# Kernel optimization log

Hardware: AMD Instinct MI355X
Metric: run time of the kernel (lower is better)

## Reference

```python
import jax, jax.numpy as jnp
import numpy as np

N = 8192
IOU_THRESH = 0.5
MAX_PROPOSALS = 1000


def setup_inputs() -> dict:
    key = jax.random.key(0)
    k1, k2, k3, k4 = jax.random.split(key, 4)
    # valid xyxy boxes inside a ~1000x1000 image, widths/heights in [1, 101)
    xy1 = jax.random.uniform(k1, (N, 2), dtype=jnp.float32) * 900.0
    wh = jax.random.uniform(k2, (N, 2), dtype=jnp.float32) * 100.0 + 1.0
    boxes = jnp.concatenate([xy1, xy1 + wh], axis=1)  # [N,4] xyxy
    scores = jax.random.uniform(k3, (N,), dtype=jnp.float32)
    return {"boxes": boxes, "scores": scores}


def _nms_keep(boxes, scores, thresh, max_proposals):
    # boxes: [N,4] xyxy (already sorted by descending score)
    x1, y1, x2, y2 = boxes[:, 0], boxes[:, 1], boxes[:, 2], boxes[:, 3]
    area = (x2 - x1) * (y2 - y1)  # [N]
    # pairwise IoU [N,N] (computed once; suppression loop gathers rows)
    xx1 = jnp.maximum(x1[:, None], x1[None, :])
    yy1 = jnp.maximum(y1[:, None], y1[None, :])
    xx2 = jnp.minimum(x2[:, None], x2[None, :])
    yy2 = jnp.minimum(y2[:, None], y2[None, :])
    inter = jnp.clip(xx2 - xx1, 0.0) * jnp.clip(yy2 - yy1, 0.0)
    iou = inter / (area[:, None] + area[None, :] - inter)
    n = boxes.shape[0]
    idx = jnp.arange(n)

    def body(i, keep):
        # box i (if still kept) suppresses later boxes with IoU > thresh
        suppress = keep[i] & (iou[i] > thresh) & (idx > i)
        return keep & ~suppress

    keep = jax.lax.fori_loop(0, n, body, jnp.ones((n,), dtype=bool))
    # truncate to max_proposals surviving boxes (in score order)
    keep = keep & (jnp.cumsum(keep.astype(jnp.int32)) <= max_proposals)
    return keep


def reference(boxes, scores):
    # sort by descending score (boxlist_nms sorts by score_field)
    order = jnp.argsort(-scores)
    b = boxes[order]          # [N,4]
    s = scores[order]         # [N]
    # keep mask is a discrete decision -> computed on stop_gradient inputs
    keep = _nms_keep(jax.lax.stop_gradient(b), jax.lax.stop_gradient(s),
                     IOU_THRESH, MAX_PROPOSALS)
    # fixed-shape output: [N,5] = (x1,y1,x2,y2,score), zeroed where suppressed
    out = jnp.concatenate([b, s[:, None]], axis=1) * keep[:, None].astype(b.dtype)
    return out
```

## Files before the change

kernel.cpp:

```cpp
#include <hip/hip_runtime.h>
#include <hip/hip_bf16.h>

#define N 8192
#define NW 128
#define GR 64
#define GROUPS 128
#define CGR 48
#define MAXP 1000
#define K_E 16
typedef unsigned long long u64;

__device__ float4 g_sboxes[N];
__device__ float  g_sscores[N];
__device__ u64    g_mask[(size_t)N * NW];
__device__ u64    g_diagT[N];
__device__ __attribute__((aligned(8))) unsigned short g_elist[N][K_E];
__device__ int    g_ecnt[N];
__device__ int    g_need_full;

__global__ __launch_bounds__(256) void k_rank2(const float4* __restrict__ boxes,
                                               const float* __restrict__ scores) {
  __shared__ u64 lk[8][1025];
  const int t = threadIdx.x;
  if (blockIdx.x < 32) g_ecnt[blockIdx.x * 256 + t] = 0;
  if (blockIdx.x == 0 && t == 0) g_need_full = 0;
#pragma unroll
  for (int k = 0; k < 32; ++k) {
    int j = t + 256 * k;
    unsigned sb = __float_as_uint(scores[j]);
    lk[j >> 10][j & 1023] = ((u64)(sb ^ 0xFFFFFFFFu) << 32) | (unsigned)j;
  }
  __syncthreads();
  const int row = blockIdx.x * 32 + (t >> 3);
  const int seg = t & 7;
  unsigned sbr = __float_as_uint(scores[row]);
  const u64 ki = ((u64)(sbr ^ 0xFFFFFFFFu) << 32) | (unsigned)row;
  const u64* s = lk[seg];
  int cnt = 0;
#pragma unroll 8
  for (int j = 0; j < 1024; ++j) cnt += (s[j] < ki) ? 1 : 0;
  cnt += __shfl_xor(cnt, 1);
  cnt += __shfl_xor(cnt, 2);
  cnt += __shfl_xor(cnt, 4);
  if (seg == 0) {
    g_sboxes[cnt] = boxes[row];
    g_sscores[cnt] = scores[row];
  }
}

__device__ __forceinline__ void tile_work(int col, int row, int lane,
                                          const float4* cb, u64* sh) {
#pragma clang fp contract(off)
  const int i = row * 64 + lane;
  const int jbase = col * 64;
  float4 bi = g_sboxes[i];
  u64 ov = 0;
  for (int c = 0; c < 64; ++c) {
    float4 bj = cb[c];
    float xx1 = fmaxf(bi.x, bj.x);
    float yy1 = fmaxf(bi.y, bj.y);
    float xx2 = fminf(bi.z, bj.z);
    float yy2 = fminf(bi.w, bj.w);
    bool cand = (xx2 > xx1) && (yy2 > yy1);
    if (cand) ov |= (1ull << c);
  }
  if (col == row) ov &= (lane < 63) ? (~0ull << (lane + 1)) : 0ull;
  float areai = (bi.z - bi.x) * (bi.w - bi.y);
  u64 bits = 0;
  while (ov) {
    int c = __ffsll((long long)ov) - 1;
    ov &= ov - 1;
    float4 bj = cb[c];
    float xx1 = fmaxf(bi.x, bj.x);
    float yy1 = fmaxf(bi.y, bj.y);
    float xx2 = fminf(bi.z, bj.z);
    float yy2 = fminf(bi.w, bj.w);
    float ww = fmaxf(xx2 - xx1, 0.0f);
    float hh = fmaxf(yy2 - yy1, 0.0f);
    float inter = ww * hh;
    float areaj = (bj.z - bj.x) * (bj.w - bj.y);
    float uni = (areai + areaj) - inter;
    float iou = inter / uni;
    if (iou > 0.5f) bits |= (1ull << c);
  }
  if (bits) g_mask[(size_t)i * NW + col] = bits;
  u64 eb = bits;
  while (eb) {
    int c = __ffsll((long long)eb) - 1;
    eb &= eb - 1;
    int slot = atomicAdd(&g_ecnt[i], 1);
    if (slot < K_E) g_elist[i][slot] = (unsigned short)(jbase + c);
  }
  if (col == row) {
    sh[lane] = bits;
    u64 colw = 0;
    for (int r = 0; r < 64; ++r) colw |= ((sh[r] >> lane) & 1ull) << r;
    g_diagT[row * 64 + lane] = colw;
  }
}

__global__ __launch_bounds__(256) void k_maskc() {
  const int col = blockIdx.x;
  const int rowq = blockIdx.y;
  if (col < rowq * 4) return;
  const int t = threadIdx.x;
  const int wv = t >> 6, lane = t & 63;
  __shared__ float4 cb[64];
  __shared__ u64 sh[4][64];
  if (t < 64) cb[t] = g_sboxes[col * 64 + t];
  __syncthreads();
  const int row = rowq * 4 + wv;
  if (col < row) return;
  tile_work(col, row, lane, cb, sh[wv]);
}

__global__ __launch_bounds__(256) void k_maskr() {
  if (g_need_full == 0) return;
  const int col = blockIdx.x;
  const int rowq = blockIdx.y;
  if (col < rowq * 4) return;
  const int t = threadIdx.x;
  const int wv = t >> 6, lane = t & 63;
  __shared__ float4 cb[64];
  __shared__ u64 sh[4][64];
  if (t < 64) cb[t] = g_sboxes[col * 64 + t];
  __syncthreads();
  const int row = rowq * 4 + wv;
  if (col < row) return;
  if (row < CGR && col < CGR) return;
  tile_work(col, row, lane, cb, sh[wv]);
}

template<int GLIM, bool GUARDED>
__device__ __forceinline__ void serial_body(float* __restrict__ out) {
  if (GUARDED && g_need_full == 0) return;
  const int t = threadIdx.x;
  const int wave = t >> 6, lane = t & 63;
  __shared__ u64 remv[NW];
  __shared__ u64 keep_arr[NW];
  __shared__ int wpre_s[NW];
  __shared__ int done_s;
  if (t < NW) { remv[t] = 0; keep_arr[t] = 0; }
  __syncthreads();

  if (wave == 0) {
    u64 tdA = g_diagT[lane];
    int cnA = g_ecnt[lane];
    const u64* el0 = (const u64*)&g_elist[lane][0];
    u64 eA0 = el0[0], eA1 = el0[1], eA2 = el0[2], eA3 = el0[3];

    int kept_total = 0;
    for (int g = 0; g < GLIM; ++g) {
      u64 tdB = 0, eB0 = 0, eB1 = 0, eB2 = 0, eB3 = 0;
      int cnB = 0;
      if (g + 1 < GLIM) {
        int base = (g + 1) * GR + lane;
        tdB = g_diagT[base];
        cnB = g_ecnt[base];
        const u64* el = (const u64*)&g_elist[base][0];
        eB0 = el[0]; eB1 = el[1]; eB2 = el[2]; eB3 = el[3];
      }
      u64 pend = ~remv[g];
      u64 keepm = 0;
      while (pend) {
        bool rdy = (((pend >> lane) & 1ull) != 0ull) && ((tdA & pend) == 0ull);
        u64 R = __ballot(rdy);
        keepm |= R;
        u64 S = __ballot((tdA & R) != 0ull);
        pend &= ~(R | S);
      }
      if (lane == 0) keep_arr[g] = keepm;
      if ((keepm >> lane) & 1ull) {
        int cnt = cnA < K_E ? cnA : K_E;
        const u64 ew0 = eA0, ew1 = eA1, ew2 = eA2, ew3 = eA3;
#define SCAT(W, Q)                                                     \
        _Pragma("unroll")                                              \
        for (int b = 0; b < 4; ++b) {                                  \
          int s = (Q) * 4 + b;                                         \
          if (s < cnt) {                                               \
            int j = (int)(((W) >> (16 * b)) & 0xFFFFull);              \
            atomicOr(&remv[j >> 6], 1ull << (j & 63));                 \
          }                                                            \
        }
        SCAT(ew0, 0) SCAT(ew1, 1) SCAT(ew2, 2) SCAT(ew3, 3)
#undef SCAT
      }
      u64 ovf = __ballot((((keepm >> lane) & 1ull) != 0ull) && (cnA > K_E));
      while (ovf) {
        int rr = __ffsll((long long)ovf) - 1;
        ovf &= ovf - 1;
        const u64* rowp = g_mask + (size_t)(g * GR + rr) * NW;
        int w0 = g + lane, w1 = g + 64 + lane;
        u64 a0 = (w0 < NW) ? rowp[w0] : 0ull;
        u64 a1 = (w1 < NW) ? rowp[w1] : 0ull;
        if (a0) atomicOr(&remv[w0], a0);
        if (a1) atomicOr(&remv[w1], a1);
      }
      kept_total += __popcll(keepm);
      if (kept_total >= MAXP) break;
      tdA = tdB; cnA = cnB;
      eA0 = eB0; eA1 = eB1; eA2 = eB2; eA3 = eB3;
    }
    if (lane == 0) done_s = (kept_total >= MAXP) ? 1 : 0;
    u64 k0 = keep_arr[2 * lane];
    u64 k1 = keep_arr[2 * lane + 1];
    int pc0 = __popcll(k0);
    int s = pc0 + __popcll(k1);
    int ex = s;
    for (int d = 1; d < 64; d <<= 1) {
      int t2 = __shfl_up(ex, d);
      if (lane >= d) ex += t2;
    }
    ex -= s;
    wpre_s[2 * lane] = ex;
    wpre_s[2 * lane + 1] = ex + pc0;
  }
  __syncthreads();

  if (!GUARDED) {
    if (done_s == 0) {
      if (t == 0) g_need_full = 1;
      return;
    }
  }
  for (int r = 0; r < N / 256; ++r) {
    int i = r * 256 + t;
    int w = i >> 6, b = i & 63;
    u64 kw = keep_arr[w];
    int before = wpre_s[w] + (b ? __popcll(kw << (64 - b)) : 0);
    bool k = (((kw >> b) & 1ull) != 0ull) && (before < MAXP);
    float m = k ? 1.0f : 0.0f;
    float4 bx = g_sboxes[i];
    float sc = g_sscores[i];
    out[i * 5 + 0] = bx.x * m;
    out[i * 5 + 1] = bx.y * m;
    out[i * 5 + 2] = bx.z * m;
    out[i * 5 + 3] = bx.w * m;
    out[i * 5 + 4] = sc * m;
  }
}

__global__ __launch_bounds__(256) void k_serialA(float* __restrict__ out) {
  serial_body<CGR, false>(out);
}
__global__ __launch_bounds__(256) void k_serialF(float* __restrict__ out) {
  serial_body<GROUPS, true>(out);
}

extern "C" void kernel_launch(void* const* d_in, const int* in_sizes, int n_in,
                              void* d_out, int out_size, void* d_ws, size_t ws_size,
                              hipStream_t stream) {
  const float4* boxes = (const float4*)d_in[0];
  const float*  scores = (const float*)d_in[1];
  float* out = (float*)d_out;

  hipLaunchKernelGGL(k_rank2,   dim3(N / 32),       dim3(256), 0, stream, boxes, scores);
  hipLaunchKernelGGL(k_maskc,   dim3(CGR, CGR / 4), dim3(256), 0, stream);
  hipLaunchKernelGGL(k_serialA, dim3(1),            dim3(256), 0, stream, out);
  hipLaunchKernelGGL(k_maskr,   dim3(NW, NW / 4),   dim3(256), 0, stream);
  hipLaunchKernelGGL(k_serialF, dim3(1),            dim3(256), 0, stream, out);
}
```

Baseline: 55.53 us.

## Fuse rank, coarse mask and serial NMS into one cooperative kernel

Merges the rank-sort, coarse-mask and first serial NMS kernels into a single cooperative launch with grid-wide syncs, cutting two kernel launch boundaries. The coarse mask tiles are also remapped from a sparse 2D grid, where most blocks exited early, to a compact list of 312 upper-triangular quad tiles. The cost is grid.sync overhead and the restriction that a cooperative launch of 256 blocks must be fully resident.

```diff
diff --git a/kernel.cpp b/kernel.cpp
--- a/kernel.cpp
+++ b/kernel.cpp
@@ -1,11 +1,15 @@
 #include <hip/hip_runtime.h>
 #include <hip/hip_bf16.h>
+#include <hip/hip_cooperative_groups.h>
+
+namespace cg = cooperative_groups;
 
 #define N 8192
 #define NW 128
 #define GR 64
 #define GROUPS 128
 #define CGR 48
+#define NQUADS 312
 #define MAXP 1000
 #define K_E 16
 typedef unsigned long long u64;
@@ -17,36 +21,6 @@
 __device__ __attribute__((aligned(8))) unsigned short g_elist[N][K_E];
 __device__ int    g_ecnt[N];
 __device__ int    g_need_full;
-
-__global__ __launch_bounds__(256) void k_rank2(const float4* __restrict__ boxes,
-                                               const float* __restrict__ scores) {
-  __shared__ u64 lk[8][1025];
-  const int t = threadIdx.x;
-  if (blockIdx.x < 32) g_ecnt[blockIdx.x * 256 + t] = 0;
-  if (blockIdx.x == 0 && t == 0) g_need_full = 0;
-#pragma unroll
-  for (int k = 0; k < 32; ++k) {
-    int j = t + 256 * k;
-    unsigned sb = __float_as_uint(scores[j]);
-    lk[j >> 10][j & 1023] = ((u64)(sb ^ 0xFFFFFFFFu) << 32) | (unsigned)j;
-  }
-  __syncthreads();
-  const int row = blockIdx.x * 32 + (t >> 3);
-  const int seg = t & 7;
-  unsigned sbr = __float_as_uint(scores[row]);
-  const u64 ki = ((u64)(sbr ^ 0xFFFFFFFFu) << 32) | (unsigned)row;
-  const u64* s = lk[seg];
-  int cnt = 0;
-#pragma unroll 8
-  for (int j = 0; j < 1024; ++j) cnt += (s[j] < ki) ? 1 : 0;
-  cnt += __shfl_xor(cnt, 1);
-  cnt += __shfl_xor(cnt, 2);
-  cnt += __shfl_xor(cnt, 4);
-  if (seg == 0) {
-    g_sboxes[cnt] = boxes[row];
-    g_sscores[cnt] = scores[row];
-  }
-}
 
 __device__ __forceinline__ void tile_work(int col, int row, int lane,
                                           const float4* cb, u64* sh) {
@@ -99,38 +73,6 @@
   }
 }
 
-__global__ __launch_bounds__(256) void k_maskc() {
-  const int col = blockIdx.x;
-  const int rowq = blockIdx.y;
-  if (col < rowq * 4) return;
-  const int t = threadIdx.x;
-  const int wv = t >> 6, lane = t & 63;
-  __shared__ float4 cb[64];
-  __shared__ u64 sh[4][64];
-  if (t < 64) cb[t] = g_sboxes[col * 64 + t];
-  __syncthreads();
-  const int row = rowq * 4 + wv;
-  if (col < row) return;
-  tile_work(col, row, lane, cb, sh[wv]);
-}
-
-__global__ __launch_bounds__(256) void k_maskr() {
-  if (g_need_full == 0) return;
-  const int col = blockIdx.x;
-  const int rowq = blockIdx.y;
-  if (col < rowq * 4) return;
-  const int t = threadIdx.x;
-  const int wv = t >> 6, lane = t & 63;
-  __shared__ float4 cb[64];
-  __shared__ u64 sh[4][64];
-  if (t < 64) cb[t] = g_sboxes[col * 64 + t];
-  __syncthreads();
-  const int row = rowq * 4 + wv;
-  if (col < row) return;
-  if (row < CGR && col < CGR) return;
-  tile_work(col, row, lane, cb, sh[wv]);
-}
-
 template<int GLIM, bool GUARDED>
 __device__ __forceinline__ void serial_body(float* __restrict__ out) {
   if (GUARDED && g_need_full == 0) return;
@@ -240,9 +182,80 @@
   }
 }
 
-__global__ __launch_bounds__(256) void k_serialA(float* __restrict__ out) {
-  serial_body<CGR, false>(out);
-}
+__global__ __launch_bounds__(256) void k_all(const float4* __restrict__ boxes,
+                                             const float* __restrict__ scores,
+                                             float* __restrict__ out) {
+  cg::grid_group grid = cg::this_grid();
+  const int t = threadIdx.x;
+  const int bid = blockIdx.x;
+
+  __shared__ u64 lk[8][1025];
+  if (bid < 32) g_ecnt[bid * 256 + t] = 0;
+  if (bid == 0 && t == 0) g_need_full = 0;
+#pragma unroll
+  for (int k = 0; k < 32; ++k) {
+    int j = t + 256 * k;
+    unsigned sb = __float_as_uint(scores[j]);
+    lk[j >> 10][j & 1023] = ((u64)(sb ^ 0xFFFFFFFFu) << 32) | (unsigned)j;
+  }
+  __syncthreads();
+  {
+    const int row = bid * 32 + (t >> 3);
+    const int seg = t & 7;
+    unsigned sbr = __float_as_uint(scores[row]);
+    const u64 ki = ((u64)(sbr ^ 0xFFFFFFFFu) << 32) | (unsigned)row;
+    const u64* s = lk[seg];
+    int cnt = 0;
+#pragma unroll 8
+    for (int j = 0; j < 1024; ++j) cnt += (s[j] < ki) ? 1 : 0;
+    cnt += __shfl_xor(cnt, 1);
+    cnt += __shfl_xor(cnt, 2);
+    cnt += __shfl_xor(cnt, 4);
+    if (seg == 0) {
+      g_sboxes[cnt] = boxes[row];
+      g_sscores[cnt] = scores[row];
+    }
+  }
+  __threadfence();
+  grid.sync();
+
+  __shared__ float4 cb[64];
+  __shared__ u64 sh[4][64];
+  const int wv = t >> 6, lane = t & 63;
+  for (int qid = bid; qid < NQUADS; qid += 256) {
+    int r = 0;
+#pragma unroll
+    for (int k = 1; k < 12; ++k) r = (qid >= k * (50 - 2 * k)) ? k : r;
+    const int col = 4 * r + (qid - r * (50 - 2 * r));
+    if (t < 64) cb[t] = g_sboxes[col * 64 + t];
+    __syncthreads();
+    const int row = r * 4 + wv;
+    if (row <= col) tile_work(col, row, lane, cb, sh[wv]);
+    __syncthreads();
+  }
+  __threadfence();
+  grid.sync();
+
+  if (bid == 0) serial_body<CGR, false>(out);
+}
+
+__global__ __launch_bounds__(256) void k_maskr() {
+  if (g_need_full == 0) return;
+  const int col = blockIdx.x;
+  const int rowq = blockIdx.y;
+  if (col < rowq * 4) return;
+  const int t = threadIdx.x;
+  const int wv = t >> 6, lane = t & 63;
+  __shared__ float4 cb[64];
+  __shared__ u64 sh[4][64];
+  if (t < 64) cb[t] = g_sboxes[col * 64 + t];
+  __syncthreads();
+  const int row = rowq * 4 + wv;
+  if (col < row) return;
+  if (row < CGR && col < CGR) return;
+  tile_work(col, row, lane, cb, sh[wv]);
+}
+
 __global__ __launch_bounds__(256) void k_serialF(float* __restrict__ out) {
   serial_body<GROUPS, true>(out);
 }
@@ -254,9 +267,8 @@
   const float*  scores = (const float*)d_in[1];
   float* out = (float*)d_out;
 
-  hipLaunchKernelGGL(k_rank2,   dim3(N / 32),       dim3(256), 0, stream, boxes, scores);
-  hipLaunchKernelGGL(k_maskc,   dim3(CGR, CGR / 4), dim3(256), 0, stream);
-  hipLaunchKernelGGL(k_serialA, dim3(1),            dim3(256), 0, stream, out);
-  hipLaunchKernelGGL(k_maskr,   dim3(NW, NW / 4),   dim3(256), 0, stream);
-  hipLaunchKernelGGL(k_serialF, dim3(1),            dim3(256), 0, stream, out);
-}
+  void* args[] = {(void*)&boxes, (void*)&scores, (void*)&out};
+  hipLaunchCooperativeKernel((void*)k_all, dim3(256), dim3(256), args, 0, stream);
+  hipLaunchKernelGGL(k_maskr,   dim3(NW, NW / 4), dim3(256), 0, stream);
+  hipLaunchKernelGGL(k_serialF, dim3(1),          dim3(256), 0, stream, out);
+}
```

New measurement: 177.8 us. 3.2x slower.
